# Performance work log

Hardware: AMD Instinct MI355X
Metric: run time of the kernel (lower is better)

## Reference

```python
import jax, jax.numpy as jnp
import numpy as np

FEATS = 1024
HEAD = 16
MLP_HIDDEN = 4096
HEAD_DIM = FEATS // HEAD
SQRT_D = float(FEATS) ** 0.5  # module scales by sqrt(feats), not sqrt(head_dim)
LN_EPS = 1e-5


def layer_norm(x, g, b):
    mu = jnp.mean(x, axis=-1, keepdims=True)
    var = jnp.mean(jnp.square(x - mu), axis=-1, keepdims=True)
    return (x - mu) * jax.lax.rsqrt(var + LN_EPS) * g + b


def setup_inputs() -> dict:
    key = jax.random.key(0)
    ks = jax.random.split(key, 12)
    s = 1.0 / np.sqrt(FEATS)
    s2 = 1.0 / np.sqrt(MLP_HIDDEN)
    return {
        "x": jax.random.normal(ks[0], (2, 2048, FEATS), dtype=jnp.float32),
        "ln1_g": jnp.ones((FEATS,), jnp.float32),
        "ln1_b": jnp.zeros((FEATS,), jnp.float32),
        "wq": jax.random.normal(ks[1], (FEATS, FEATS), jnp.float32) * s,
        "bq": jnp.zeros((FEATS,), jnp.float32),
        "wk": jax.random.normal(ks[2], (FEATS, FEATS), jnp.float32) * s,
        "bk": jnp.zeros((FEATS,), jnp.float32),
        "wv": jax.random.normal(ks[3], (FEATS, FEATS), jnp.float32) * s,
        "bv": jnp.zeros((FEATS,), jnp.float32),
        "wo": jax.random.normal(ks[4], (FEATS, FEATS), jnp.float32) * s,
        "bo": jnp.zeros((FEATS,), jnp.float32),
        "ln2_g": jnp.ones((FEATS,), jnp.float32),
        "ln2_b": jnp.zeros((FEATS,), jnp.float32),
        "w1": jax.random.normal(ks[5], (MLP_HIDDEN, FEATS), jnp.float32) * s,
        "b1": jnp.zeros((MLP_HIDDEN,), jnp.float32),
        "w2": jax.random.normal(ks[6], (FEATS, MLP_HIDDEN), jnp.float32) * s2,
        "b2": jnp.zeros((FEATS,), jnp.float32),
    }


def reference(x, ln1_g, ln1_b, wq, bq, wk, bk, wv, bv, wo, bo,
              ln2_g, ln2_b, w1, b1, w2, b2):
    b, n, f = x.shape
    h = layer_norm(x, ln1_g, ln1_b)
    # qkv projections (torch Linear: y = x @ W.T + b)
    q = (h @ wq.T + bq).reshape(b, n, HEAD, HEAD_DIM).transpose(0, 2, 1, 3)
    k = (h @ wk.T + bk).reshape(b, n, HEAD, HEAD_DIM).transpose(0, 2, 1, 3)
    v = (h @ wv.T + bv).reshape(b, n, HEAD, HEAD_DIM).transpose(0, 2, 1, 3)
    score = jax.nn.softmax(jnp.einsum('bhif,bhjf->bhij', q, k) / SQRT_D, axis=-1)
    attn = jnp.einsum('bhij,bhjf->bihf', score, v).reshape(b, n, f)
    o = attn @ wo.T + bo
    out1 = o + x
    h2 = layer_norm(out1, ln2_g, ln2_b)
    mlp = jax.nn.relu(jax.nn.relu(h2 @ w1.T + b1) @ w2.T + b2)
    return mlp + out1
```

## Files before the change

### kernel.cpp

```cpp
#include <hip/hip_runtime.h>
#include <hip/hip_bf16.h>

#define FEATS 1024
#define NH 16
#define HD 64
#define SEQ 2048
#define BATCH 2
#define MTOT (BATCH*SEQ)
#define MLPH 4096
#define QSCALE 0.04508422277369218f

typedef __attribute__((ext_vector_type(8))) short bf16x8;
typedef __attribute__((ext_vector_type(4))) short bf16x4;
typedef __attribute__((ext_vector_type(4))) float f32x4;

static_assert(sizeof(bf16x8) == 16, "bf16x8 must be 16B");

__device__ __forceinline__ unsigned short f2bf(float f) {
    unsigned int u = __float_as_uint(f);
    unsigned int lsb = (u >> 16) & 1u;
    u += 0x7fffu + lsb;
    return (unsigned short)(u >> 16);
}

#define ASYNC16(GP, LP) __builtin_amdgcn_global_load_lds( \
    (const __attribute__((address_space(1))) void*)(GP),  \
    (__attribute__((address_space(3))) void*)(LP), 16, 0, 0)

#define WAIT_VM(N) asm volatile("s_waitcnt vmcnt(" #N ")" ::: "memory")

__global__ __launch_bounds__(256) void cvt_all_kernel(
    const float* __restrict__ wq, const float* __restrict__ wk,
    const float* __restrict__ wv, const float* __restrict__ wo,
    const float* __restrict__ w1, const float* __restrict__ w2,
    unsigned short* __restrict__ dst) {
    const size_t i = ((size_t)blockIdx.x * 256 + threadIdx.x) * 4;
    const size_t MB = (size_t)1024 * 1024;
    const float* s;
    size_t off;
    float sc = 1.0f;
    if (i < MB)            { s = wq; off = i;          sc = QSCALE; }
    else if (i < 2 * MB)   { s = wk; off = i - MB; }
    else if (i < 3 * MB)   { s = wv; off = i - 2 * MB; }
    else if (i < 4 * MB)   { s = wo; off = i - 3 * MB; }
    else if (i < 8 * MB)   { s = w1; off = i - 4 * MB; }
    else                   { s = w2; off = i - 8 * MB; }
    float4 v = *(const float4*)(s + off);
    ushort4 o;
    o.x = f2bf(v.x * sc); o.y = f2bf(v.y * sc);
    o.z = f2bf(v.z * sc); o.w = f2bf(v.w * sc);
    *(ushort4*)(dst + i) = o;
}

__global__ __launch_bounds__(256) void concat3_kernel(const float* __restrict__ a,
                                                      const float* __restrict__ b,
                                                      const float* __restrict__ c,
                                                      float* __restrict__ o) {
    int i = blockIdx.x * 256 + threadIdx.x;
    float v = (i < 1024) ? a[i] * QSCALE : ((i < 2048) ? b[i - 1024] : c[i - 2048]);
    o[i] = v;
}

__global__ __launch_bounds__(256) void ln_kernel(const float* __restrict__ x,
                                                 const float* __restrict__ g,
                                                 const float* __restrict__ bta,
                                                 unsigned short* __restrict__ h) {
    __shared__ float red[8];
    const int row = blockIdx.x;
    const int t = threadIdx.x;
    const float* xr = x + (size_t)row * FEATS;
    float4 v = ((const float4*)xr)[t];
    float s  = v.x + v.y + v.z + v.w;
    float ss = v.x * v.x + v.y * v.y + v.z * v.z + v.w * v.w;
#pragma unroll
    for (int off = 1; off < 64; off <<= 1) {
        s  += __shfl_xor(s, off);
        ss += __shfl_xor(ss, off);
    }
    const int w = t >> 6;
    if ((t & 63) == 0) { red[w] = s; red[4 + w] = ss; }
    __syncthreads();
    s  = red[0] + red[1] + red[2] + red[3];
    ss = red[4] + red[5] + red[6] + red[7];
    const float mu  = s * (1.f / FEATS);
    const float var = ss * (1.f / FEATS) - mu * mu;
    const float rs  = rsqrtf(var + 1e-5f);
    float4 gv = ((const float4*)g)[t];
    float4 bv = ((const float4*)bta)[t];
    ushort4 ov;
    ov.x = f2bf((v.x - mu) * rs * gv.x + bv.x);
    ov.y = f2bf((v.y - mu) * rs * gv.y + bv.y);
    ov.z = f2bf((v.z - mu) * rs * gv.z + bv.z);
    ov.w = f2bf((v.w - mu) * rs * gv.w + bv.w);
    ((ushort4*)h)[(size_t)row * (FEATS / 4) + t] = ov;
}

template <int DEPTH, bool RELU, bool ADD, bool OUTBF16>
__global__ __launch_bounds__(256, (DEPTH == 3 ? 3 : 2))
void gemm_kernel(const unsigned short* __restrict__ A,
                 const unsigned short* __restrict__ W,
                 const float* __restrict__ bias,
                 const float* __restrict__ addend,
                 void* __restrict__ outp,
                 int M, int N, int K, int gx) {
    __shared__ unsigned short lds[DEPTH][2][128 * 32];

    const int t = threadIdx.x;
    const int w = t >> 6, lane = t & 63;
    const int wr = w >> 1, wc = w & 1;
    const int li = lane & 15, lj = lane >> 4;

    const int nwg = gridDim.x;
    const int cpx = nwg >> 3;
    const int wg = blockIdx.x;
    const int swz = (wg & 7) * cpx + (wg >> 3);
    const int mb = (swz / gx) * 128, nb = (swz % gx) * 128;

    const int srow = lane >> 2;
    const int scg = ((lane & 3) ^ (srow & 3)) * 8;
    const unsigned short* gA = A + (size_t)(mb + w * 16 + srow) * K + scg;
    const unsigned short* gB = W + (size_t)(nb + w * 16 + srow) * K + scg;
    const size_t half = (size_t)64 * K;
    const int lbase = w * 512 + lane * 8;

    const int rsw = (lj ^ (li & 3)) * 8;

    const int nt = K >> 5;

#define STAGE(BUF, K0)                                             \
    do {                                                           \
        unsigned short* la_ = &lds[BUF][0][lbase];                 \
        unsigned short* lb_ = &lds[BUF][1][lbase];                 \
        ASYNC16(gA + (K0), la_);                                   \
        ASYNC16(gA + half + (K0), la_ + 2048);                     \
        ASYNC16(gB + (K0), lb_);                                   \
        ASYNC16(gB + half + (K0), lb_ + 2048);                     \
    } while (0)

#pragma unroll
    for (int j = 0; j < DEPTH - 1; ++j)
        STAGE(j, j * 32);
    if constexpr (DEPTH == 3) WAIT_VM(4); else WAIT_VM(8);
    __builtin_amdgcn_s_barrier();

    f32x4 acc[4][4] = {};

    for (int i = 0; i < nt; ++i) {
        const int cur = i % DEPTH;
        const unsigned short* Al = &lds[cur][0][0];
        const unsigned short* Bl = &lds[cur][1][0];

        bf16x8 af[4], bfr[4];
#pragma unroll
        for (int m = 0; m < 4; m++)
            af[m] = *(const bf16x8*)(Al + (wr * 64 + m * 16 + li) * 32 + rsw);
#pragma unroll
        for (int n = 0; n < 4; n++)
            bfr[n] = *(const bf16x8*)(Bl + (wc * 64 + n * 16 + li) * 32 + rsw);

        const int pft = i + DEPTH - 1;
        if (pft < nt) STAGE(pft % DEPTH, pft * 32);

#pragma unroll
        for (int m = 0; m < 4; m++)
#pragma unroll
            for (int n = 0; n < 4; n++)
                acc[m][n] = __builtin_amdgcn_mfma_f32_16x16x32_bf16(af[m], bfr[n], acc[m][n], 0, 0, 0);

        if (i + 1 < nt) {
            const int avail = (nt - 2) - i;
            const int rem = avail < (DEPTH - 2) ? avail : (DEPTH - 2);
            if (rem >= DEPTH - 2) { if constexpr (DEPTH == 3) WAIT_VM(4); else WAIT_VM(8); }
            else if (rem == 1) WAIT_VM(4);
            else               WAIT_VM(0);
            __builtin_amdgcn_s_barrier();
        }
    }
#undef STAGE

#pragma unroll
    for (int m = 0; m < 4; m++) {
#pragma unroll
        for (int n = 0; n < 4; n++) {
            const int col = nb + wc * 64 + n * 16 + li;
            const float bv = bias[col];
#pragma unroll
            for (int r = 0; r < 4; r++) {
                const int row = mb + wr * 64 + m * 16 + lj * 4 + r;
                float v = acc[m][n][r] + bv;
                if (RELU) v = fmaxf(v, 0.f);
                if (ADD)  v += addend[(size_t)row * N + col];
                if (OUTBF16)
                    ((unsigned short*)outp)[(size_t)row * N + col] = f2bf(v);
                else
                    ((float*)outp)[(size_t)row * N + col] = v;
            }
        }
    }
}

__global__ __launch_bounds__(256) void vtrans_kernel(const unsigned short* __restrict__ qkv,
                                                     unsigned short* __restrict__ vt) {
    constexpr int LDV = 68;
    __shared__ unsigned short Vl[64 * LDV];
    const int bh = blockIdx.x, st = blockIdx.y;
    const int b = bh >> 4, h = bh & 15;
    const int t = threadIdx.x;
    const unsigned short* src = qkv + (size_t)(b * SEQ + st * 64) * (3 * FEATS) + 2 * FEATS + h * HD;
#pragma unroll
    for (int i = 0; i < 2; i++) {
        int idx = t + i * 256;
        int r = idx >> 3, c = (idx & 7) * 8;
        *(bf16x8*)(Vl + r * LDV + c) = *(const bf16x8*)(src + (size_t)r * (3 * FEATS) + c);
    }
    __syncthreads();
    unsigned short* dst = vt + (size_t)bh * HD * SEQ + st * 64;
#pragma unroll
    for (int i = 0; i < 2; i++) {
        int idx = t + i * 256;
        int d = idx >> 3, s8 = (idx & 7) * 8;
        const int base = s8 & ~31;
        const int u4 = ((s8 >> 3) & 3) * 4;
        bf16x8 v;
#pragma unroll
        for (int j = 0; j < 8; j++) {
            const int key = base + u4 + (j & 3) + ((j >> 2) & 1) * 16;
            v[j] = Vl[key * LDV + d];
        }
        *(bf16x8*)(dst + (size_t)d * SEQ + s8) = v;
    }
}

__global__ __launch_bounds__(256, 4)
void attn_kernel(const unsigned short* __restrict__ qkv,
                 const unsigned short* __restrict__ vt,
                 unsigned short* __restrict__ out) {
    constexpr int LK = 72;
    __shared__ unsigned short Kl[2][64 * LK];
    __shared__ unsigned short Vtl[2][64 * LK];

    const int bh = blockIdx.x;
    const int b = bh >> 4, h = bh & 15;
    const int q0 = blockIdx.y * 128;
    const int t = threadIdx.x, w = t >> 6, lane = t & 63;
    const int li = lane & 15, lj = lane >> 4;

    const size_t rstr = 3 * FEATS;
    const unsigned short* qkvb = qkv + (size_t)(b * SEQ) * rstr;
    const unsigned short* ksrc = qkvb + FEATS + h * HD;
    const unsigned short* vsrc = vt + (size_t)bh * HD * SEQ;

    bf16x8 aq[2][2];
#pragma unroll
    for (int hh = 0; hh < 2; hh++)
#pragma unroll
        for (int kk = 0; kk < 2; kk++)
            aq[hh][kk] = *(const bf16x8*)(qkvb +
                (size_t)(q0 + w * 32 + hh * 16 + li) * rstr + h * HD + kk * 32 + lj * 8);

    f32x4 o[2][4] = {};
    f32x4 oS[2] = {};

    const short onebf = (short)0x3F80;
    const bf16x8 ones = {onebf, onebf, onebf, onebf, onebf, onebf, onebf, onebf};

    const int sr = t >> 2, sc = (t & 3) * 16;
    const unsigned short* kg = ksrc + (size_t)sr * rstr + sc;
    const unsigned short* vg = vsrc + (size_t)sr * SEQ + sc;
    const int ldo = sr * LK + sc;

    const int nt = SEQ / 64;

    {
        bf16x8 k0 = *(const bf16x8*)kg;
        bf16x8 k1 = *(const bf16x8*)(kg + 8);
        bf16x8 v0 = *(const bf16x8*)vg;
        bf16x8 v1 = *(const bf16x8*)(vg + 8);
        *(bf16x8*)(&Kl[0][ldo])      = k0;
        *(bf16x8*)(&Kl[0][ldo + 8])  = k1;
        *(bf16x8*)(&Vtl[0][ldo])     = v0;
        *(bf16x8*)(&Vtl[0][ldo + 8]) = v1;
    }

    int cur = 0;
    for (int i = 0; i < nt; ++i) {
        bf16x8 kr0, kr1, vr0, vr1;
        if (i + 1 < nt) {
            const unsigned short* kn = kg + (size_t)(i + 1) * 64 * rstr;
            const unsigned short* vn = vg + (i + 1) * 64;
            kr0 = *(const bf16x8*)kn;
            kr1 = *(const bf16x8*)(kn + 8);
            vr0 = *(const bf16x8*)vn;
            vr1 = *(const bf16x8*)(vn + 8);
        }

        asm volatile("s_waitcnt lgkmcnt(0)" ::: "memory");
        __builtin_amdgcn_s_barrier();

        const unsigned short* Kc = Kl[cur];
        const unsigned short* Vc = Vtl[cur];

        f32x4 s[2][4];
        __builtin_amdgcn_s_setprio(1);
#pragma unroll
        for (int n = 0; n < 4; n++) {
            bf16x8 k0 = *(const bf16x8*)(Kc + (n * 16 + li) * LK + lj * 8);
            bf16x8 k1 = *(const bf16x8*)(Kc + (n * 16 + li) * LK + 32 + lj * 8);
#pragma unroll
            for (int hh = 0; hh < 2; hh++) {
                f32x4 acc = {};
                acc = __builtin_amdgcn_mfma_f32_16x16x32_bf16(k0, aq[hh][0], acc, 0, 0, 0);
                acc = __builtin_amdgcn_mfma_f32_16x16x32_bf16(k1, aq[hh][1], acc, 0, 0, 0);
                s[hh][n] = acc;
            }
        }
        __builtin_amdgcn_s_setprio(0);

        bf16x8 A[2][2];
#pragma unroll
        for (int hh = 0; hh < 2; hh++)
#pragma unroll
            for (int kk = 0; kk < 2; kk++) {
                float p[8];
#pragma unroll
                for (int r = 0; r < 4; r++) {
                    p[r]     = exp2f(s[hh][2 * kk][r]);
                    p[4 + r] = exp2f(s[hh][2 * kk + 1][r]);
                }
                union { unsigned u[4]; bf16x8 v; } Au;
                asm("v_cvt_pk_bf16_f32 %0, %1, %2" : "=v"(Au.u[0]) : "v"(p[0]), "v"(p[1]));
                asm("v_cvt_pk_bf16_f32 %0, %1, %2" : "=v"(Au.u[1]) : "v"(p[2]), "v"(p[3]));
                asm("v_cvt_pk_bf16_f32 %0, %1, %2" : "=v"(Au.u[2]) : "v"(p[4]), "v"(p[5]));
                asm("v_cvt_pk_bf16_f32 %0, %1, %2" : "=v"(Au.u[3]) : "v"(p[6]), "v"(p[7]));
                A[hh][kk] = Au.v;
            }

#pragma unroll
        for (int hh = 0; hh < 2; hh++)
#pragma unroll
            for (int kk = 0; kk < 2; kk++)
                oS[hh] = __builtin_amdgcn_mfma_f32_16x16x32_bf16(A[hh][kk], ones, oS[hh], 0, 0, 0);

        __builtin_amdgcn_s_setprio(1);
#pragma unroll
        for (int n = 0; n < 4; n++) {
#pragma unroll
            for (int kk = 0; kk < 2; kk++) {
                bf16x8 bv = *(const bf16x8*)(Vc + (n * 16 + li) * LK + kk * 32 + lj * 8);
                o[0][n] = __builtin_amdgcn_mfma_f32_16x16x32_bf16(A[0][kk], bv, o[0][n], 0, 0, 0);
                o[1][n] = __builtin_amdgcn_mfma_f32_16x16x32_bf16(A[1][kk], bv, o[1][n], 0, 0, 0);
            }
        }
        __builtin_amdgcn_s_setprio(0);

        if (i + 1 < nt) {
            *(bf16x8*)(&Kl[cur ^ 1][ldo])      = kr0;
            *(bf16x8*)(&Kl[cur ^ 1][ldo + 8])  = kr1;
            *(bf16x8*)(&Vtl[cur ^ 1][ldo])     = vr0;
            *(bf16x8*)(&Vtl[cur ^ 1][ldo + 8]) = vr1;
        }
        cur ^= 1;
    }

    unsigned short* ob = out + (size_t)(b * SEQ + q0 + w * 32) * FEATS + h * HD;
#pragma unroll
    for (int hh = 0; hh < 2; hh++)
#pragma unroll
        for (int r = 0; r < 4; r++) {
            const float inv = 1.f / oS[hh][r];
#pragma unroll
            for (int n = 0; n < 4; n++)
                ob[(size_t)(hh * 16 + lj * 4 + r) * FEATS + n * 16 + li] =
                    f2bf(o[hh][n][r] * inv);
        }
}

extern "C" void kernel_launch(void* const* d_in, const int* in_sizes, int n_in,
                              void* d_out, int out_size, void* d_ws, size_t ws_size,
                              hipStream_t stream) {
    const float* x     = (const float*)d_in[0];
    const float* ln1_g = (const float*)d_in[1];
    const float* ln1_b = (const float*)d_in[2];
    const float* wq    = (const float*)d_in[3];
    const float* bq    = (const float*)d_in[4];
    const float* wk    = (const float*)d_in[5];
    const float* bk    = (const float*)d_in[6];
    const float* wv    = (const float*)d_in[7];
    const float* bvv   = (const float*)d_in[8];
    const float* wo    = (const float*)d_in[9];
    const float* bo    = (const float*)d_in[10];
    const float* ln2_g = (const float*)d_in[11];
    const float* ln2_b = (const float*)d_in[12];
    const float* w1    = (const float*)d_in[13];
    const float* b1    = (const float*)d_in[14];
    const float* w2    = (const float*)d_in[15];
    const float* b2    = (const float*)d_in[16];

    unsigned short* wqkv_b = (unsigned short*)d_ws;
    unsigned short* wo_b   = wqkv_b + 3072 * 1024;
    unsigned short* w1_b   = wo_b + 1024 * 1024;
    unsigned short* w2_b   = w1_b + 4096 * 1024;
    float*          bqkv   = (float*)(w2_b + 1024 * 4096);
    unsigned short* region = (unsigned short*)(bqkv + 3072);
    unsigned short* qkvb   = region;
    unsigned short* hb     = region + (size_t)4096 * 3072;
    unsigned short* vtb    = hb;
    unsigned short* a1     = region;
    unsigned short* attn_o = region + (size_t)4096 * 4096;
    unsigned short* h2     = attn_o;
    float*          out1   = (float*)(attn_o + (size_t)4096 * 1024);
    float*          outf   = (float*)d_out;

    dim3 blk(256);

    cvt_all_kernel<<<12288, blk, 0, stream>>>(wq, wk, wv, wo, w1, w2, wqkv_b);
    concat3_kernel<<<12, blk, 0, stream>>>(bq, bk, bvv, bqkv);

    ln_kernel<<<MTOT, blk, 0, stream>>>(x, ln1_g, ln1_b, hb);

    gemm_kernel<3, false, false, true><<<768, blk, 0, stream>>>(
        hb, wqkv_b, bqkv, nullptr, qkvb, MTOT, 3072, FEATS, 24);

    vtrans_kernel<<<dim3(BATCH * NH, SEQ / 64), blk, 0, stream>>>(qkvb, vtb);

    attn_kernel<<<dim3(BATCH * NH, SEQ / 128), dim3(256), 0, stream>>>(qkvb, vtb, attn_o);

    gemm_kernel<4, false, true, false><<<256, blk, 0, stream>>>(
        attn_o, wo_b, bo, x, out1, MTOT, FEATS, FEATS, 8);

    ln_kernel<<<MTOT, blk, 0, stream>>>(out1, ln2_g, ln2_b, h2);

    gemm_kernel<3, true, false, true><<<1024, blk, 0, stream>>>(
        h2, w1_b, b1, nullptr, a1, MTOT, MLPH, FEATS, 32);

    gemm_kernel<4, true, true, false><<<256, blk, 0, stream>>>(
        a1, w2_b, b2, out1, outf, MTOT, FEATS, MLPH, 8);
}
```

Measured before the change: 232.2 us.

## Split-K the MLP down-projection and store the residual stream in bf16

The final MLP GEMM (K=4096), which launched only 256 workgroups, is now split in two along K via blockIdx.z. Each half writes fp32 partials, and a new combine kernel sums them and applies bias, ReLU and the residual add. This is meant to fill more CUs on the long-K GEMM. The out1 residual is also stored as bf16 instead of fp32 and read back by a templated LayerNorm, cutting memory traffic. In exchange, the residual loses precision and the change adds an extra kernel plus fp32 partial write/read traffic.

Measured after the change: 233.4 us. About the same (+0.5%).

```diff
diff --git a/kernel.cpp b/kernel.cpp
--- a/kernel.cpp
+++ b/kernel.cpp
@@ -11,7 +11,6 @@
 #define QSCALE 0.04508422277369218f
 
 typedef __attribute__((ext_vector_type(8))) short bf16x8;
-typedef __attribute__((ext_vector_type(4))) short bf16x4;
 typedef __attribute__((ext_vector_type(4))) float f32x4;
 
 static_assert(sizeof(bf16x8) == 16, "bf16x8 must be 16B");
@@ -21,6 +20,9 @@
     unsigned int lsb = (u >> 16) & 1u;
     u += 0x7fffu + lsb;
     return (unsigned short)(u >> 16);
+}
+__device__ __forceinline__ float bf2f(unsigned short u) {
+    return __uint_as_float((unsigned)u << 16);
 }
 
 #define ASYNC16(GP, LP) __builtin_amdgcn_global_load_lds( \
@@ -61,15 +63,23 @@
     o[i] = v;
 }
 
-__global__ __launch_bounds__(256) void ln_kernel(const float* __restrict__ x,
+template <bool INBF16>
+__global__ __launch_bounds__(256) void ln_kernel(const void* __restrict__ xin,
                                                  const float* __restrict__ g,
                                                  const float* __restrict__ bta,
                                                  unsigned short* __restrict__ h) {
     __shared__ float red[8];
     const int row = blockIdx.x;
     const int t = threadIdx.x;
-    const float* xr = x + (size_t)row * FEATS;
-    float4 v = ((const float4*)xr)[t];
+    float4 v;
+    if (INBF16) {
+        const unsigned short* xr = (const unsigned short*)xin + (size_t)row * FEATS;
+        ushort4 u = ((const ushort4*)xr)[t];
+        v.x = bf2f(u.x); v.y = bf2f(u.y); v.z = bf2f(u.z); v.w = bf2f(u.w);
+    } else {
+        const float* xr = (const float*)xin + (size_t)row * FEATS;
+        v = ((const float4*)xr)[t];
+    }
     float s  = v.x + v.y + v.z + v.w;
     float ss = v.x * v.x + v.y * v.y + v.z * v.z + v.w * v.w;
 #pragma unroll
@@ -95,13 +105,14 @@
     ((ushort4*)h)[(size_t)row * (FEATS / 4) + t] = ov;
 }
 
-template <int DEPTH, bool RELU, bool ADD, bool OUTBF16>
+template <int DEPTH, bool RELU, bool ADDF32, bool OUTBF16, bool SPLITK>
 __global__ __launch_bounds__(256, (DEPTH == 3 ? 3 : 2))
 void gemm_kernel(const unsigned short* __restrict__ A,
                  const unsigned short* __restrict__ W,
                  const float* __restrict__ bias,
                  const float* __restrict__ addend,
                  void* __restrict__ outp,
+                 float* __restrict__ ps1,
                  int M, int N, int K, int gx) {
     __shared__ unsigned short lds[DEPTH][2][128 * 32];
 
@@ -116,16 +127,19 @@
     const int swz = (wg & 7) * cpx + (wg >> 3);
     const int mb = (swz / gx) * 128, nb = (swz % gx) * 128;
 
+    const int kbase = SPLITK ? (int)blockIdx.z * (K >> 1) : 0;
+    const int klen  = SPLITK ? (K >> 1) : K;
+
     const int srow = lane >> 2;
     const int scg = ((lane & 3) ^ (srow & 3)) * 8;
-    const unsigned short* gA = A + (size_t)(mb + w * 16 + srow) * K + scg;
-    const unsigned short* gB = W + (size_t)(nb + w * 16 + srow) * K + scg;
+    const unsigned short* gA = A + (size_t)(mb + w * 16 + srow) * K + kbase + scg;
+    const unsigned short* gB = W + (size_t)(nb + w * 16 + srow) * K + kbase + scg;
     const size_t half = (size_t)64 * K;
     const int lbase = w * 512 + lane * 8;
 
     const int rsw = (lj ^ (li & 3)) * 8;
 
-    const int nt = K >> 5;
+    const int nt = klen >> 5;
 
 #define STAGE(BUF, K0)                                             \
     do {                                                           \
@@ -178,25 +192,49 @@
     }
 #undef STAGE
 
+    float* psdst = nullptr;
+    if (SPLITK) psdst = (blockIdx.z == 0) ? (float*)outp : ps1;
+
 #pragma unroll
     for (int m = 0; m < 4; m++) {
 #pragma unroll
         for (int n = 0; n < 4; n++) {
             const int col = nb + wc * 64 + n * 16 + li;
-            const float bv = bias[col];
+            const float bv = SPLITK ? 0.f : bias[col];
 #pragma unroll
             for (int r = 0; r < 4; r++) {
                 const int row = mb + wr * 64 + m * 16 + lj * 4 + r;
                 float v = acc[m][n][r] + bv;
-                if (RELU) v = fmaxf(v, 0.f);
-                if (ADD)  v += addend[(size_t)row * N + col];
-                if (OUTBF16)
-                    ((unsigned short*)outp)[(size_t)row * N + col] = f2bf(v);
-                else
-                    ((float*)outp)[(size_t)row * N + col] = v;
+                if (SPLITK) {
+                    psdst[(size_t)row * N + col] = acc[m][n][r];
+                } else {
+                    if (RELU) v = fmaxf(v, 0.f);
+                    if (ADDF32) v += addend[(size_t)row * N + col];
+                    if (OUTBF16)
+                        ((unsigned short*)outp)[(size_t)row * N + col] = f2bf(v);
+                    else
+                        ((float*)outp)[(size_t)row * N + col] = v;
+                }
             }
         }
     }
+}
+
+__global__ __launch_bounds__(256) void mlp2_combine_kernel(
+    const float* __restrict__ ps0, const float* __restrict__ ps1,
+    const float* __restrict__ b2, const unsigned short* __restrict__ out1b,
+    float* __restrict__ out) {
+    const int row = blockIdx.x, t = threadIdx.x;
+    float4 p0 = ((const float4*)(ps0 + (size_t)row * FEATS))[t];
+    float4 p1 = ((const float4*)(ps1 + (size_t)row * FEATS))[t];
+    float4 bb = ((const float4*)b2)[t];
+    ushort4 o1 = ((const ushort4*)(out1b + (size_t)row * FEATS))[t];
+    float4 ov;
+    ov.x = fmaxf(p0.x + p1.x + bb.x, 0.f) + bf2f(o1.x);
+    ov.y = fmaxf(p0.y + p1.y + bb.y, 0.f) + bf2f(o1.y);
+    ov.z = fmaxf(p0.z + p1.z + bb.z, 0.f) + bf2f(o1.z);
+    ov.w = fmaxf(p0.w + p1.w + bb.w, 0.f) + bf2f(o1.w);
+    ((float4*)(out + (size_t)row * FEATS))[t] = ov;
 }
 
 __global__ __launch_bounds__(256) void vtrans_kernel(const unsigned short* __restrict__ qkv,
@@ -396,19 +434,22 @@
     const float* w2    = (const float*)d_in[15];
     const float* b2    = (const float*)d_in[16];
 
-    unsigned short* wqkv_b = (unsigned short*)d_ws;
-    unsigned short* wo_b   = wqkv_b + 3072 * 1024;
-    unsigned short* w1_b   = wo_b + 1024 * 1024;
-    unsigned short* w2_b   = w1_b + 4096 * 1024;
-    float*          bqkv   = (float*)(w2_b + 1024 * 4096);
-    unsigned short* region = (unsigned short*)(bqkv + 3072);
-    unsigned short* qkvb   = region;
-    unsigned short* hb     = region + (size_t)4096 * 3072;
+    constexpr size_t MBs = 512 * 1024;
+    unsigned short* ws16   = (unsigned short*)d_ws;
+    unsigned short* wqkv_b = ws16;
+    unsigned short* wo_b   = ws16 + 6 * MBs;
+    unsigned short* w1_b   = ws16 + 8 * MBs;
+    unsigned short* w2_b   = ws16 + 16 * MBs;
+    float*          bqkv   = (float*)(ws16 + 24 * MBs);
+    unsigned short* attn_o = ws16 + 24 * MBs;
+    unsigned short* h2     = ws16 + 32 * MBs;
+    unsigned short* qkvb   = ws16 + 40 * MBs;
+    unsigned short* hb     = ws16 + 64 * MBs;
     unsigned short* vtb    = hb;
-    unsigned short* a1     = region;
-    unsigned short* attn_o = region + (size_t)4096 * 4096;
-    unsigned short* h2     = attn_o;
-    float*          out1   = (float*)(attn_o + (size_t)4096 * 1024);
+    unsigned short* a1     = ws16 + 40 * MBs;
+    unsigned short* out1b  = ws16 + 72 * MBs;
+    float*          ps0    = (float*)ws16;
+    float*          ps1    = (float*)(ws16 + 24 * MBs);
     float*          outf   = (float*)d_out;
 
     dim3 blk(256);
@@ -416,23 +457,25 @@
     cvt_all_kernel<<<12288, blk, 0, stream>>>(wq, wk, wv, wo, w1, w2, wqkv_b);
     concat3_kernel<<<12, blk, 0, stream>>>(bq, bk, bvv, bqkv);
 
-    ln_kernel<<<MTOT, blk, 0, stream>>>(x, ln1_g, ln1_b, hb);
-
-    gemm_kernel<3, false, false, true><<<768, blk, 0, stream>>>(
-        hb, wqkv_b, bqkv, nullptr, qkvb, MTOT, 3072, FEATS, 24);
+    ln_kernel<false><<<MTOT, blk, 0, stream>>>(x, ln1_g, ln1_b, hb);
+
+    gemm_kernel<3, false, false, true, false><<<768, blk, 0, stream>>>(
+        hb, wqkv_b, bqkv, nullptr, qkvb, nullptr, MTOT, 3072, FEATS, 24);
 
     vtrans_kernel<<<dim3(BATCH * NH, SEQ / 64), blk, 0, stream>>>(qkvb, vtb);
 
-    attn_kernel<<<dim3(BATCH * NH, SEQ / 128), dim3(256), 0, stream>>>(qkvb, vtb, attn_o);
-
-    gemm_kernel<4, false, true, false><<<256, blk, 0, stream>>>(
-        attn_o, wo_b, bo, x, out1, MTOT, FEATS, FEATS, 8);
-
-    ln_kernel<<<MTOT, blk, 0, stream>>>(out1, ln2_g, ln2_b, h2);
-
-    gemm_kernel<3, true, false, true><<<1024, blk, 0, stream>>>(
-        h2, w1_b, b1, nullptr, a1, MTOT, MLPH, FEATS, 32);
-
-    gemm_kernel<4, true, true, false><<<256, blk, 0, stream>>>(
-        a1, w2_b, b2, out1, outf, MTOT, FEATS, MLPH, 8);
-}
+    attn_kernel<<<dim3(BATCH * NH, SEQ / 128), blk, 0, stream>>>(qkvb, vtb, attn_o);
+
+    gemm_kernel<4, false, true, true, false><<<256, blk, 0, stream>>>(
+        attn_o, wo_b, bo, x, out1b, nullptr, MTOT, FEATS, FEATS, 8);
+
+    ln_kernel<true><<<MTOT, blk, 0, stream>>>(out1b, ln2_g, ln2_b, h2);
+
+    gemm_kernel<3, true, false, true, false><<<1024, blk, 0, stream>>>(
+        h2, w1_b, b1, nullptr, a1, nullptr, MTOT, MLPH, FEATS, 32);
+
+    gemm_kernel<4, false, false, false, true><<<dim3(256, 1, 2), blk, 0, stream>>>(
+        a1, w2_b, nullptr, nullptr, ps0, ps1, MTOT, FEATS, MLPH, 8);
+
+    mlp2_combine_kernel<<<MTOT, blk, 0, stream>>>(ps0, ps1, b2, out1b, outf);
+}
```
